# Performance work log

Hardware: AMD Instinct MI355X
Metric: run time of the kernel (lower is better)

## Reference

```python
import jax, jax.numpy as jnp
import numpy as np

# ---- configuration matching init_kwargs ----
KH, KW = 3, 3
STRIDE = (1, 1)
PAD = (1, 1)
DIL = (1, 1)
GRID_SIZE = 5
SPLINE_ORDER = 3
GRID_RANGE = (-1.0, 1.0)
CIN, COUT = 16, 32
B, H, W = 16, 64, 64
K = KH * KW                      # in_features of each KANLinear
NB = GRID_SIZE + SPLINE_ORDER    # number of B-spline basis functions / coeffs


def make_grid():
    # efficient-KAN style extended uniform knot vector, shared by all units
    h = (GRID_RANGE[1] - GRID_RANGE[0]) / GRID_SIZE
    return (jnp.arange(-SPLINE_ORDER, GRID_SIZE + SPLINE_ORDER + 1,
                       dtype=jnp.float32) * h + GRID_RANGE[0])  # [G + 2k + 1]


def setup_inputs() -> dict:
    key = jax.random.key(0)
    k1, k2, k3, k4 = jax.random.split(key, 4)
    n_convs = COUT * CIN  # one KANLinear per (out_channel, in_channel) pair
    x = jax.random.normal(k1, (B, CIN, H, W), dtype=jnp.float32)
    base_w = jax.random.normal(k2, (n_convs, K), dtype=jnp.float32) * (1.0 / np.sqrt(K))
    spline_w = jax.random.normal(k3, (n_convs, K, NB), dtype=jnp.float32) * 0.1
    spline_scaler = jax.random.normal(k4, (n_convs, K), dtype=jnp.float32) * (1.0 / np.sqrt(K))
    return {"x": x, "base_w": base_w, "spline_w": spline_w,
            "spline_scaler": spline_scaler}


def extract_patches(x):
    # im2col / torch.nn.Unfold: [B, Cin, H, W] -> [B, Cin, Ho, Wo, K]
    xp = jnp.pad(x, ((0, 0), (0, 0), (PAD[0], PAD[0]), (PAD[1], PAD[1])))
    Hp, Wp = xp.shape[2], xp.shape[3]
    Ho = (Hp - DIL[0] * (KH - 1) - 1) // STRIDE[0] + 1
    Wo = (Wp - DIL[1] * (KW - 1) - 1) // STRIDE[1] + 1
    cols = []
    for i in range(KH):          # tiny fixed kernel loop (9 iters)
        for j in range(KW):
            cols.append(xp[:, :,
                           i * DIL[0]: i * DIL[0] + STRIDE[0] * Ho: STRIDE[0],
                           j * DIL[1]: j * DIL[1] + STRIDE[1] * Wo: STRIDE[1]])
    return jnp.stack(cols, axis=-1)  # [B, Cin, Ho, Wo, K]


def bspline_bases(x, t):
    # Cox-de Boor recursion, vectorized over all leading dims.
    # x: [...], t: [G+2k+1] shared knots -> bases [..., NB]
    xe = x[..., None]
    b = ((xe >= t[:-1]) & (xe < t[1:])).astype(x.dtype)
    for p in range(1, SPLINE_ORDER + 1):
        left = (xe - t[:-(p + 1)]) / (t[p:-1] - t[:-(p + 1)]) * b[..., :-1]
        right = (t[p + 1:] - xe) / (t[p + 1:] - t[1:-p]) * b[..., 1:]
        b = left + right
    return b  # [..., NB]


def reference(x, base_w, spline_w, spline_scaler):
    t = make_grid()
    patches = extract_patches(x)                 # [B, Cin, Ho, Wo, K]
    act = jax.nn.silu(patches)                   # base branch activation
    bases = bspline_bases(patches, t)            # [B, Cin, Ho, Wo, K, NB]
    # KANLinear list ordering: kernel index = c_out * Cin + c_in
    bw = base_w.reshape(COUT, CIN, K)
    sw = (spline_w * spline_scaler[..., None]).reshape(COUT, CIN, K, NB)
    # out[b,o,h,w] = sum_i KANLinear_{o,i}(patch[b,i,h,w,:])
    out = jnp.einsum('bihwk,oik->bohw', act, bw)
    out = out + jnp.einsum('bihwkc,oikc->bohw', bases, sw)
    return out
```

## Files before the change

kernel.cpp:

```cpp
#include <hip/hip_runtime.h>
#include <hip/hip_bf16.h>

#define CIN_ 16
#define COUT_ 32
#define NBATCH_ 16
#define H_ 64
#define W_ 64
#define F_ 10
#define LPIX_ 336
#define PXT_ 34
#define LROWT_ (PXT_ * LPIX_)
#define ROWS_ 6
#define NSITE_ (ROWS_ * PXT_)
#define NIT_ 13

typedef __attribute__((ext_vector_type(8))) short short8;
typedef __attribute__((ext_vector_type(4))) float f32x4;

__device__ __forceinline__ unsigned short f2bf(float f) {
    unsigned u = __builtin_bit_cast(unsigned, f);
    u += 0x7FFFu + ((u >> 16) & 1u);
    return (unsigned short)(u >> 16);
}
__device__ __forceinline__ unsigned pack2(float lo, float hi) {
    return (unsigned)f2bf(lo) | ((unsigned)f2bf(hi) << 16);
}

__global__ void kan_packw(const float* __restrict__ bw, const float* __restrict__ sw,
                          const float* __restrict__ sc, unsigned short* __restrict__ wpk) {
    int e = blockIdx.x * 256 + threadIdx.x;
    if (e >= 32 * 16 * 9) return;
    int n = e / 144;
    int ci = (e / 9) & 15;
    int tap = e % 9;
    float bwv = bw[e];
    float scv = sc[e];
    float4 s0 = *(const float4*)(sw + (size_t)e * 8);
    float4 s1 = *(const float4*)(sw + (size_t)e * 8 + 4);
    float swv[8] = {s0.x, s0.y, s0.z, s0.w, s1.x, s1.y, s1.z, s1.w};
    int nt = n >> 4, nl = n & 15;
#pragma unroll
    for (int f = 0; f < 10; ++f) {
        float v = (f == 0) ? bwv : (f <= 8 ? swv[f - 1] * scv : 0.0f);
        int k = ci * 10 + f;
        int c = k >> 5, r = k & 31;
        int lane = ((r >> 3) << 4) | nl;
        int j = r & 7;
        size_t off = ((size_t)(((tap * 2 + nt) * 5 + c) * 64 + lane)) * 8 + j;
        wpk[off] = f2bf(v);
    }
}

__global__ __launch_bounds__(256, 2) void kan_fused(const float* __restrict__ x,
                                                    const unsigned short* __restrict__ wpk,
                                                    float* __restrict__ out) {
    __shared__ __align__(16) char lA[ROWS_ * LROWT_];
    int tid = threadIdx.x;
    int bb = blockIdx.x >> 5;
    int rem = blockIdx.x & 31;
    int rg = rem >> 1;
    int wseg = rem & 1;
    int h0 = rg * 4;
    int w0 = wseg * 32;

    {
        int ci = tid >> 4;
        int l = tid & 15;
        const float* xb = x + ((size_t)bb * CIN_ + ci) * (H_ * W_);
        float xr[NIT_];
#pragma unroll
        for (int it = 0; it < NIT_; ++it) {
            int s = it * 16 + l;
            int r = s / PXT_;
            int lpx = s - r * PXT_;
            int hy = h0 + r - 1;
            int wx = w0 + lpx - 1;
            bool v = (s < NSITE_) && (hy >= 0) && (hy < H_) && (wx >= 0) && (wx < W_);
            xr[it] = v ? xb[hy * W_ + wx] : 0.f;
        }
#pragma unroll
        for (int it = 0; it < NIT_; ++it) {
            int s = it * 16 + l;
            if (s < NSITE_) {
                int r = s / PXT_;
                int lpx = s - r * PXT_;
                float xv = xr[it];
                float ua = (xv + 2.2f) * 2.5f;
                float mf = floorf(ua);
                float u = ua - mf;
                bool ok = (ua >= 0.0f) && (ua < 11.0f);
                float u2 = u * u, u3 = u2 * u;
                const float c6 = 1.0f / 6.0f;
                float Bm  = u3 * c6;
                float Bm1 = (-3.f * u3 + 3.f * u2 + 3.f * u + 1.f) * c6;
                float Bm2 = (3.f * u3 - 6.f * u2 + 4.f) * c6;
                float om = 1.f - u;
                float Bm3 = om * om * om * c6;
                unsigned P0 = pack2(Bm3, Bm2);
                unsigned P1 = pack2(Bm1, Bm);
                int sh = ok ? ((int)mf - 2) : 99;
                int a = sh >> 1;
                bool odd = sh & 1;
                unsigned Q0 = odd ? (P0 << 16) : P0;
                unsigned Q1 = odd ? ((P0 >> 16) | (P1 << 16)) : P1;
                unsigned Q2 = odd ? (P1 >> 16) : 0u;
                unsigned wq[5];
#pragma unroll
                for (int q = 0; q < 5; ++q)
                    wq[q] = (q == a) ? Q0 : (q == a + 1) ? Q1 : (q == a + 2) ? Q2 : 0u;
                float sil = xv / (1.f + __expf(-xv));
                wq[0] = (wq[0] & 0xFFFF0000u) | (unsigned)f2bf(sil);
                unsigned* dst = (unsigned*)(lA + r * LROWT_ + lpx * LPIX_ + ci * 20);
#pragma unroll
                for (int q = 0; q < 5; ++q) dst[q] = wq[q];
            }
        }
    }

    int lane = tid & 63, wv = tid >> 6;
    int lrow = lane & 15, khalf = lane >> 4;
    int p = wv & 1;
    int nt = wv >> 1;

    short8 B[2][5];
#pragma unroll
    for (int c = 0; c < 5; ++c)
        B[0][c] = *(const short8*)(wpk + (size_t)((nt * 5 + c) * 64 + lane) * 8);

    __syncthreads();

    f32x4 acc[4];
#pragma unroll
    for (int mi = 0; mi < 4; ++mi) acc[mi] = (f32x4){0.f, 0.f, 0.f, 0.f};

#pragma unroll
    for (int tap = 0; tap < 9; ++tap) {
        int cur = tap & 1, nxt = cur ^ 1;
        if (tap < 8) {
#pragma unroll
            for (int c = 0; c < 5; ++c)
                B[nxt][c] = *(const short8*)(wpk +
                    (size_t)((((tap + 1) * 2 + nt) * 5 + c) * 64 + lane) * 8);
        }
        int ki = tap / 3, kj = tap - ki * 3;
        const char* abase = lA + (2 * p + ki) * LROWT_ + (lrow + kj) * LPIX_ + khalf * 16;
        __builtin_amdgcn_s_setprio(1);
#pragma unroll
        for (int c = 0; c < 5; ++c) {
            short8 a0 = *(const short8*)(abase + c * 64);
            short8 a1 = *(const short8*)(abase + 16 * LPIX_ + c * 64);
            short8 a2 = *(const short8*)(abase + LROWT_ + c * 64);
            short8 a3 = *(const short8*)(abase + LROWT_ + 16 * LPIX_ + c * 64);
            acc[0] = __builtin_amdgcn_mfma_f32_16x16x32_bf16(a0, B[cur][c], acc[0], 0, 0, 0);
            acc[1] = __builtin_amdgcn_mfma_f32_16x16x32_bf16(a1, B[cur][c], acc[1], 0, 0, 0);
            acc[2] = __builtin_amdgcn_mfma_f32_16x16x32_bf16(a2, B[cur][c], acc[2], 0, 0, 0);
            acc[3] = __builtin_amdgcn_mfma_f32_16x16x32_bf16(a3, B[cur][c], acc[3], 0, 0, 0);
        }
        __builtin_amdgcn_s_setprio(0);
    }

    int ch = nt * 16 + lrow;
    float* ob = out + (size_t)bb * COUT_ * (H_ * W_) + (size_t)ch * (H_ * W_);
#pragma unroll
    for (int mi = 0; mi < 4; ++mi) {
        int hh = h0 + 2 * p + (mi >> 1);
        int px = w0 + (mi & 1) * 16 + khalf * 4;
        __builtin_nontemporal_store(acc[mi], (f32x4*)(ob + (size_t)hh * W_ + px));
    }
}

__device__ __forceinline__ void kan_feat10_ref(float xv, float* f) {
    float ua = (xv + 2.2f) * 2.5f;
    float mf = floorf(ua);
    int m = (int)mf;
    float u = ua - mf;
    bool ok = (ua >= 0.0f) && (ua < 11.0f);
    float u2 = u * u, u3 = u2 * u;
    const float c6 = 1.0f / 6.0f;
    float Bm  = u3 * c6;
    float Bm1 = (-3.f * u3 + 3.f * u2 + 3.f * u + 1.f) * c6;
    float Bm2 = (3.f * u3 - 6.f * u2 + 4.f) * c6;
    float om = 1.f - u;
    float Bm3 = om * om * om * c6;
    if (!ok) { Bm = 0.f; Bm1 = 0.f; Bm2 = 0.f; Bm3 = 0.f; }
    f[0] = xv / (1.f + __expf(-xv));
#pragma unroll
    for (int j = 0; j < 8; ++j) {
        float v = 0.f;
        v = (m == j)     ? Bm  : v;
        v = (m == j + 1) ? Bm1 : v;
        v = (m == j + 2) ? Bm2 : v;
        v = (m == j + 3) ? Bm3 : v;
        f[1 + j] = v;
    }
    f[9] = 0.f;
}

__global__ void kan_direct(const float* __restrict__ x, const float* __restrict__ bw,
                           const float* __restrict__ sw, const float* __restrict__ sc,
                           float* __restrict__ out) {
    int idx = blockIdx.x * 256 + threadIdx.x;
    if (idx >= NBATCH_ * COUT_ * H_ * W_) return;
    int w = idx & 63, hh = (idx >> 6) & 63, o = (idx >> 12) & 31, b = idx >> 17;
    float acc = 0.0f;
    for (int i = 0; i < CIN_; ++i)
        for (int ki = 0; ki < 3; ++ki)
            for (int kj = 0; kj < 3; ++kj) {
                int hy = hh + ki - 1, wx = w + kj - 1;
                float xv = (hy >= 0 && hy < H_ && wx >= 0 && wx < W_)
                               ? x[(((size_t)b * CIN_ + i) * H_ + hy) * W_ + wx]
                               : 0.0f;
                float f[10];
                kan_feat10_ref(xv, f);
                int idx9 = (o * CIN_ + i) * 9 + ki * 3 + kj;
                float a = f[0] * bw[idx9];
                float s = sc[idx9];
#pragma unroll
                for (int cc = 0; cc < 8; ++cc) a += f[1 + cc] * sw[idx9 * 8 + cc] * s;
                acc += a;
            }
    out[idx] = acc;
}

extern "C" void kernel_launch(void* const* d_in, const int* in_sizes, int n_in,
                              void* d_out, int out_size, void* d_ws, size_t ws_size,
                              hipStream_t stream) {
    const float* x  = (const float*)d_in[0];
    const float* bw = (const float*)d_in[1];
    const float* sw = (const float*)d_in[2];
    const float* sc = (const float*)d_in[3];
    float* out = (float*)d_out;

    size_t need = (size_t)9 * 2 * 5 * 64 * 8 * 2;
    if (ws_size >= need) {
        unsigned short* wpk = (unsigned short*)d_ws;
        kan_packw<<<dim3(18), 256, 0, stream>>>(bw, sw, sc, wpk);
        kan_fused<<<dim3(NBATCH_ * 32), 256, 0, stream>>>(x, wpk, out);
    } else {
        kan_direct<<<dim3((NBATCH_ * COUT_ * H_ * W_ + 255) / 256), 256, 0, stream>>>(
            x, bw, sw, sc, out);
    }
}
```

Baseline: 21.58 us.

## Switch to 32x32x16 MFMA with packed 9-feature layout removing padding

Each input channel now stores 9 features instead of a zero-padded 10, so K per tap shrinks from 160 to 144. The GEMM switches from four 16x16x32 MFMAs per chunk to one 32x32x16 MFMA per step, with each wave covering all 32 output channels for one row of 32 pixels. The weight packing, LDS addressing (odd channels need unaligned halfword writes) and output store mapping are reworked to match. This cuts wasted MFMA work on padding and the LDS footprint, at the cost of more weight registers per wave and misaligned LDS writes.

Measured after the change: 21.90 us. Within noise of the previous version (+1.5%).

```diff
diff --git a/kernel.cpp b/kernel.cpp
--- a/kernel.cpp
+++ b/kernel.cpp
@@ -6,8 +6,8 @@
 #define NBATCH_ 16
 #define H_ 64
 #define W_ 64
-#define F_ 10
-#define LPIX_ 336
+#define F_ 9
+#define LPIX_ 304
 #define PXT_ 34
 #define LROWT_ (PXT_ * LPIX_)
 #define ROWS_ 6
@@ -16,6 +16,7 @@
 
 typedef __attribute__((ext_vector_type(8))) short short8;
 typedef __attribute__((ext_vector_type(4))) float f32x4;
+typedef __attribute__((ext_vector_type(16))) float f32x16;
 
 __device__ __forceinline__ unsigned short f2bf(float f) {
     unsigned u = __builtin_bit_cast(unsigned, f);
@@ -38,16 +39,14 @@
     float4 s0 = *(const float4*)(sw + (size_t)e * 8);
     float4 s1 = *(const float4*)(sw + (size_t)e * 8 + 4);
     float swv[8] = {s0.x, s0.y, s0.z, s0.w, s1.x, s1.y, s1.z, s1.w};
-    int nt = n >> 4, nl = n & 15;
-#pragma unroll
-    for (int f = 0; f < 10; ++f) {
-        float v = (f == 0) ? bwv : (f <= 8 ? swv[f - 1] * scv : 0.0f);
-        int k = ci * 10 + f;
-        int c = k >> 5, r = k & 31;
-        int lane = ((r >> 3) << 4) | nl;
+#pragma unroll
+    for (int f = 0; f < 9; ++f) {
+        float v = (f == 0) ? bwv : swv[f - 1] * scv;
+        int k = ci * 9 + f;
+        int step = k >> 4, r = k & 15;
+        int lane = ((r >> 3) << 5) | n;
         int j = r & 7;
-        size_t off = ((size_t)(((tap * 2 + nt) * 5 + c) * 64 + lane)) * 8 + j;
-        wpk[off] = f2bf(v);
+        wpk[((size_t)(tap * 9 + step) * 64 + lane) * 8 + j] = f2bf(v);
     }
 }
 
@@ -110,66 +109,68 @@
                     wq[q] = (q == a) ? Q0 : (q == a + 1) ? Q1 : (q == a + 2) ? Q2 : 0u;
                 float sil = xv / (1.f + __expf(-xv));
                 wq[0] = (wq[0] & 0xFFFF0000u) | (unsigned)f2bf(sil);
-                unsigned* dst = (unsigned*)(lA + r * LROWT_ + lpx * LPIX_ + ci * 20);
-#pragma unroll
-                for (int q = 0; q < 5; ++q) dst[q] = wq[q];
+                char* base = lA + r * LROWT_ + lpx * LPIX_ + ci * 18;
+                if ((ci & 1) == 0) {
+                    unsigned* d32 = (unsigned*)base;
+#pragma unroll
+                    for (int q = 0; q < 4; ++q) d32[q] = wq[q];
+                    ((unsigned short*)base)[8] = (unsigned short)wq[4];
+                } else {
+                    ((unsigned short*)base)[0] = (unsigned short)wq[0];
+                    unsigned* d32 = (unsigned*)(base + 2);
+#pragma unroll
+                    for (int q = 0; q < 4; ++q)
+                        d32[q] = (wq[q] >> 16) | (wq[q + 1] << 16);
+                }
             }
         }
     }
 
     int lane = tid & 63, wv = tid >> 6;
-    int lrow = lane & 15, khalf = lane >> 4;
-    int p = wv & 1;
-    int nt = wv >> 1;
-
-    short8 B[2][5];
-#pragma unroll
-    for (int c = 0; c < 5; ++c)
-        B[0][c] = *(const short8*)(wpk + (size_t)((nt * 5 + c) * 64 + lane) * 8);
+
+    short8 B[2][9];
+#pragma unroll
+    for (int s = 0; s < 9; ++s)
+        B[0][s] = *(const short8*)(wpk + ((size_t)s * 64 + lane) * 8);
 
     __syncthreads();
 
-    f32x4 acc[4];
-#pragma unroll
-    for (int mi = 0; mi < 4; ++mi) acc[mi] = (f32x4){0.f, 0.f, 0.f, 0.f};
+    f32x16 acc = {};
 
 #pragma unroll
     for (int tap = 0; tap < 9; ++tap) {
         int cur = tap & 1, nxt = cur ^ 1;
         if (tap < 8) {
 #pragma unroll
-            for (int c = 0; c < 5; ++c)
-                B[nxt][c] = *(const short8*)(wpk +
-                    (size_t)((((tap + 1) * 2 + nt) * 5 + c) * 64 + lane) * 8);
+            for (int s = 0; s < 9; ++s)
+                B[nxt][s] = *(const short8*)(wpk +
+                    ((size_t)((tap + 1) * 9 + s) * 64 + lane) * 8);
         }
         int ki = tap / 3, kj = tap - ki * 3;
-        const char* abase = lA + (2 * p + ki) * LROWT_ + (lrow + kj) * LPIX_ + khalf * 16;
+        const char* abase = lA + (wv + ki) * LROWT_ + ((lane & 31) + kj) * LPIX_ +
+                            ((lane >> 5) << 4);
         __builtin_amdgcn_s_setprio(1);
 #pragma unroll
-        for (int c = 0; c < 5; ++c) {
-            short8 a0 = *(const short8*)(abase + c * 64);
-            short8 a1 = *(const short8*)(abase + 16 * LPIX_ + c * 64);
-            short8 a2 = *(const short8*)(abase + LROWT_ + c * 64);
-            short8 a3 = *(const short8*)(abase + LROWT_ + 16 * LPIX_ + c * 64);
-            acc[0] = __builtin_amdgcn_mfma_f32_16x16x32_bf16(a0, B[cur][c], acc[0], 0, 0, 0);
-            acc[1] = __builtin_amdgcn_mfma_f32_16x16x32_bf16(a1, B[cur][c], acc[1], 0, 0, 0);
-            acc[2] = __builtin_amdgcn_mfma_f32_16x16x32_bf16(a2, B[cur][c], acc[2], 0, 0, 0);
-            acc[3] = __builtin_amdgcn_mfma_f32_16x16x32_bf16(a3, B[cur][c], acc[3], 0, 0, 0);
+        for (int s = 0; s < 9; ++s) {
+            short8 av = *(const short8*)(abase + s * 32);
+            acc = __builtin_amdgcn_mfma_f32_32x32x16_bf16(av, B[cur][s], acc, 0, 0, 0);
         }
         __builtin_amdgcn_s_setprio(0);
     }
 
-    int ch = nt * 16 + lrow;
-    float* ob = out + (size_t)bb * COUT_ * (H_ * W_) + (size_t)ch * (H_ * W_);
-#pragma unroll
-    for (int mi = 0; mi < 4; ++mi) {
-        int hh = h0 + 2 * p + (mi >> 1);
-        int px = w0 + (mi & 1) * 16 + khalf * 4;
-        __builtin_nontemporal_store(acc[mi], (f32x4*)(ob + (size_t)hh * W_ + px));
-    }
-}
-
-__device__ __forceinline__ void kan_feat10_ref(float xv, float* f) {
+    int ch = lane & 31;
+    int hh = h0 + wv;
+    float* ob = out + (size_t)bb * COUT_ * (H_ * W_) + (size_t)ch * (H_ * W_) +
+                (size_t)hh * W_ + w0;
+#pragma unroll
+    for (int q = 0; q < 4; ++q) {
+        int px0 = q * 8 + ((lane >> 5) << 2);
+        f32x4 v = {acc[q * 4 + 0], acc[q * 4 + 1], acc[q * 4 + 2], acc[q * 4 + 3]};
+        __builtin_nontemporal_store(v, (f32x4*)(ob + px0));
+    }
+}
+
+__device__ __forceinline__ void kan_feat_ref(float xv, float* f) {
     float ua = (xv + 2.2f) * 2.5f;
     float mf = floorf(ua);
     int m = (int)mf;
@@ -193,7 +194,6 @@
         v = (m == j + 3) ? Bm3 : v;
         f[1 + j] = v;
     }
-    f[9] = 0.f;
 }
 
 __global__ void kan_direct(const float* __restrict__ x, const float* __restrict__ bw,
@@ -210,8 +210,8 @@
                 float xv = (hy >= 0 && hy < H_ && wx >= 0 && wx < W_)
                                ? x[(((size_t)b * CIN_ + i) * H_ + hy) * W_ + wx]
                                : 0.0f;
-                float f[10];
-                kan_feat10_ref(xv, f);
+                float f[9];
+                kan_feat_ref(xv, f);
                 int idx9 = (o * CIN_ + i) * 9 + ki * 3 + kj;
                 float a = f[0] * bw[idx9];
                 float s = sc[idx9];
@@ -231,7 +231,7 @@
     const float* sc = (const float*)d_in[3];
     float* out = (float*)d_out;
 
-    size_t need = (size_t)9 * 2 * 5 * 64 * 8 * 2;
+    size_t need = (size_t)9 * 9 * 64 * 8 * 2;
     if (ws_size >= need) {
         unsigned short* wpk = (unsigned short*)d_ws;
         kan_packw<<<dim3(18), 256, 0, stream>>>(bw, sw, sc, wpk);
```

## Halve block tile width, double grid, and remap waves to output rows

Applied to the files above, without the earlier changes.

Each block now covers a 4x16 pixel tile instead of 4x32, so the grid doubles to 1024 blocks and LDS per block shrinks, which allows a higher launch-bounds occupancy target. Each wave now handles one output row and both 16-channel output tiles (2 accumulators), loading the B weights per tap with no double buffering. The aim is more parallelism and occupancy; the cost is a larger recomputed halo fraction for the spline features and more global weight loads per MFMA. The silu division is also swapped for a fast reciprocal.

New measurement: 28.68 us. +32.9%, slower.

```diff
diff --git a/kernel.cpp b/kernel.cpp
--- a/kernel.cpp
+++ b/kernel.cpp
@@ -8,11 +8,11 @@
 #define W_ 64
 #define F_ 10
 #define LPIX_ 336
-#define PXT_ 34
+#define PXT_ 18
 #define LROWT_ (PXT_ * LPIX_)
 #define ROWS_ 6
 #define NSITE_ (ROWS_ * PXT_)
-#define NIT_ 13
+#define NIT_ 7
 
 typedef __attribute__((ext_vector_type(8))) short short8;
 typedef __attribute__((ext_vector_type(4))) float f32x4;
@@ -46,22 +46,19 @@
         int c = k >> 5, r = k & 31;
         int lane = ((r >> 3) << 4) | nl;
         int j = r & 7;
-        size_t off = ((size_t)(((tap * 2 + nt) * 5 + c) * 64 + lane)) * 8 + j;
-        wpk[off] = f2bf(v);
-    }
-}
-
-__global__ __launch_bounds__(256, 2) void kan_fused(const float* __restrict__ x,
+        wpk[((size_t)(((tap * 2 + nt) * 5 + c)) * 64 + lane) * 8 + j] = f2bf(v);
+    }
+}
+
+__global__ __launch_bounds__(256, 4) void kan_fused(const float* __restrict__ x,
                                                     const unsigned short* __restrict__ wpk,
                                                     float* __restrict__ out) {
     __shared__ __align__(16) char lA[ROWS_ * LROWT_];
     int tid = threadIdx.x;
-    int bb = blockIdx.x >> 5;
-    int rem = blockIdx.x & 31;
-    int rg = rem >> 1;
-    int wseg = rem & 1;
-    int h0 = rg * 4;
-    int w0 = wseg * 32;
+    int bb = blockIdx.x >> 6;
+    int rem = blockIdx.x & 63;
+    int h0 = (rem >> 2) * 4;
+    int w0 = (rem & 3) * 16;
 
     {
         int ci = tid >> 4;
@@ -108,7 +105,7 @@
 #pragma unroll
                 for (int q = 0; q < 5; ++q)
                     wq[q] = (q == a) ? Q0 : (q == a + 1) ? Q1 : (q == a + 2) ? Q2 : 0u;
-                float sil = xv / (1.f + __expf(-xv));
+                float sil = xv * __builtin_amdgcn_rcpf(1.f + __expf(-xv));
                 wq[0] = (wq[0] & 0xFFFF0000u) | (unsigned)f2bf(sil);
                 unsigned* dst = (unsigned*)(lA + r * LROWT_ + lpx * LPIX_ + ci * 20);
 #pragma unroll
@@ -116,60 +113,46 @@
             }
         }
     }
+    __syncthreads();
 
     int lane = tid & 63, wv = tid >> 6;
     int lrow = lane & 15, khalf = lane >> 4;
-    int p = wv & 1;
-    int nt = wv >> 1;
-
-    short8 B[2][5];
-#pragma unroll
-    for (int c = 0; c < 5; ++c)
-        B[0][c] = *(const short8*)(wpk + (size_t)((nt * 5 + c) * 64 + lane) * 8);
-
-    __syncthreads();
-
-    f32x4 acc[4];
-#pragma unroll
-    for (int mi = 0; mi < 4; ++mi) acc[mi] = (f32x4){0.f, 0.f, 0.f, 0.f};
+
+    f32x4 acc[2] = {{0.f, 0.f, 0.f, 0.f}, {0.f, 0.f, 0.f, 0.f}};
 
 #pragma unroll
     for (int tap = 0; tap < 9; ++tap) {
-        int cur = tap & 1, nxt = cur ^ 1;
-        if (tap < 8) {
-#pragma unroll
-            for (int c = 0; c < 5; ++c)
-                B[nxt][c] = *(const short8*)(wpk +
-                    (size_t)((((tap + 1) * 2 + nt) * 5 + c) * 64 + lane) * 8);
-        }
+        short8 B[5][2];
+#pragma unroll
+        for (int c = 0; c < 5; ++c)
+#pragma unroll
+            for (int nt = 0; nt < 2; ++nt)
+                B[c][nt] = *(const short8*)(wpk +
+                    ((size_t)(((tap * 2 + nt) * 5 + c)) * 64 + lane) * 8);
         int ki = tap / 3, kj = tap - ki * 3;
-        const char* abase = lA + (2 * p + ki) * LROWT_ + (lrow + kj) * LPIX_ + khalf * 16;
+        const char* abase = lA + (wv + ki) * LROWT_ + (lrow + kj) * LPIX_ + khalf * 16;
         __builtin_amdgcn_s_setprio(1);
 #pragma unroll
         for (int c = 0; c < 5; ++c) {
-            short8 a0 = *(const short8*)(abase + c * 64);
-            short8 a1 = *(const short8*)(abase + 16 * LPIX_ + c * 64);
-            short8 a2 = *(const short8*)(abase + LROWT_ + c * 64);
-            short8 a3 = *(const short8*)(abase + LROWT_ + 16 * LPIX_ + c * 64);
-            acc[0] = __builtin_amdgcn_mfma_f32_16x16x32_bf16(a0, B[cur][c], acc[0], 0, 0, 0);
-            acc[1] = __builtin_amdgcn_mfma_f32_16x16x32_bf16(a1, B[cur][c], acc[1], 0, 0, 0);
-            acc[2] = __builtin_amdgcn_mfma_f32_16x16x32_bf16(a2, B[cur][c], acc[2], 0, 0, 0);
-            acc[3] = __builtin_amdgcn_mfma_f32_16x16x32_bf16(a3, B[cur][c], acc[3], 0, 0, 0);
+            short8 av = *(const short8*)(abase + c * 64);
+            acc[0] = __builtin_amdgcn_mfma_f32_16x16x32_bf16(av, B[c][0], acc[0], 0, 0, 0);
+            acc[1] = __builtin_amdgcn_mfma_f32_16x16x32_bf16(av, B[c][1], acc[1], 0, 0, 0);
         }
         __builtin_amdgcn_s_setprio(0);
     }
 
-    int ch = nt * 16 + lrow;
-    float* ob = out + (size_t)bb * COUT_ * (H_ * W_) + (size_t)ch * (H_ * W_);
-#pragma unroll
-    for (int mi = 0; mi < 4; ++mi) {
-        int hh = h0 + 2 * p + (mi >> 1);
-        int px = w0 + (mi & 1) * 16 + khalf * 4;
-        __builtin_nontemporal_store(acc[mi], (f32x4*)(ob + (size_t)hh * W_ + px));
-    }
-}
-
-__device__ __forceinline__ void kan_feat10_ref(float xv, float* f) {
+    int hh = h0 + wv;
+    float* ob = out + (size_t)bb * COUT_ * (H_ * W_) + (size_t)hh * W_ + w0;
+#pragma unroll
+    for (int nt = 0; nt < 2; ++nt) {
+        int och = nt * 16 + lrow;
+        f32x4 v = acc[nt];
+        __builtin_nontemporal_store(v,
+            (f32x4*)(ob + (size_t)och * (H_ * W_) + khalf * 4));
+    }
+}
+
+__device__ __forceinline__ void kan_feat_ref(float xv, float* f) {
     float ua = (xv + 2.2f) * 2.5f;
     float mf = floorf(ua);
     int m = (int)mf;
@@ -193,7 +176,6 @@
         v = (m == j + 3) ? Bm3 : v;
         f[1 + j] = v;
     }
-    f[9] = 0.f;
 }
 
 __global__ void kan_direct(const float* __restrict__ x, const float* __restrict__ bw,
@@ -210,8 +192,8 @@
                 float xv = (hy >= 0 && hy < H_ && wx >= 0 && wx < W_)
                                ? x[(((size_t)b * CIN_ + i) * H_ + hy) * W_ + wx]
                                : 0.0f;
-                float f[10];
-                kan_feat10_ref(xv, f);
+                float f[9];
+                kan_feat_ref(xv, f);
                 int idx9 = (o * CIN_ + i) * 9 + ki * 3 + kj;
                 float a = f[0] * bw[idx9];
                 float s = sc[idx9];
@@ -235,7 +217,7 @@
     if (ws_size >= need) {
         unsigned short* wpk = (unsigned short*)d_ws;
         kan_packw<<<dim3(18), 256, 0, stream>>>(bw, sw, sc, wpk);
-        kan_fused<<<dim3(NBATCH_ * 32), 256, 0, stream>>>(x, wpk, out);
+        kan_fused<<<dim3(NBATCH_ * 64), 256, 0, stream>>>(x, wpk, out);
     } else {
         kan_direct<<<dim3((NBATCH_ * COUT_ * H_ * W_ + 255) / 256), 256, 0, stream>>>(
             x, bw, sw, sc, out);
```
